# Performance work log

Hardware: AMD Instinct MI355X
Metric: run time of the kernel (lower is better)

## Reference

```python
import jax, jax.numpy as jnp
import numpy as np
from jax import lax

D = 1024      # d_model
NH = 16       # n_head
CA = 384      # adapter_channels
T = 16        # num_frames
B = 4         # videos
L = 257       # tokens = 16*16 patches + CLS
HW = 16       # spatial side


def setup_inputs() -> dict:
    key = jax.random.key(0)
    ks = jax.random.split(key, 12)
    s = 0.02
    f = lambda k, shp: jax.random.normal(k, shp, jnp.float32) * s
    return {
        'x': jax.random.normal(ks[0], (B * T, L, D), jnp.float32),
        'ln1_g': jnp.ones((D,), jnp.float32), 'ln1_b': jnp.zeros((D,), jnp.float32),
        'w_in': f(ks[1], (3 * D, D)), 'b_in': jnp.zeros((3 * D,), jnp.float32),
        'w_out': f(ks[2], (D, D)), 'b_out': jnp.zeros((D,), jnp.float32),
        'o_fc1_w': f(ks[3], (CA, D)), 'o_fc1_b': jnp.zeros((CA,), jnp.float32),
        'o_conv_w': f(ks[4], (3, 3, 1, CA)), 'o_conv_b': jnp.zeros((CA,), jnp.float32),
        'o_fc2_w': f(ks[5], (D, CA)), 'o_fc2_b': jnp.zeros((D,), jnp.float32),
        'a_fc1_w': f(ks[6], (CA, D)), 'a_fc1_b': jnp.zeros((CA,), jnp.float32),
        'a_conv_w': f(ks[7], (3, 1, CA)), 'a_conv_b': jnp.zeros((CA,), jnp.float32),
        'a_fc2_w': f(ks[8], (D, CA)), 'a_fc2_b': jnp.zeros((D,), jnp.float32),
        'ln2_g': jnp.ones((D,), jnp.float32), 'ln2_b': jnp.zeros((D,), jnp.float32),
        'mlp_fc_w': f(ks[9], (4 * D, D)), 'mlp_fc_b': jnp.zeros((4 * D,), jnp.float32),
        'mlp_proj_w': f(ks[10], (D, 4 * D)), 'mlp_proj_b': jnp.zeros((D,), jnp.float32),
    }


def _ln(x, g, b):
    # fp32 LayerNorm (matches CLIP LayerNorm subclass)
    x32 = x.astype(jnp.float32)
    mu = jnp.mean(x32, -1, keepdims=True)
    var = jnp.mean(jnp.square(x32 - mu), -1, keepdims=True)
    return ((x32 - mu) * lax.rsqrt(var + 1e-5) * g + b).astype(x.dtype)


def _mha(x, w_in, b_in, w_out, b_out):
    BT, Lq, C = x.shape
    hd = C // NH
    qkv = x @ w_in.T + b_in                       # (BT, L, 3C)
    q, k, v = jnp.split(qkv, 3, axis=-1)
    sh = lambda t: t.reshape(BT, Lq, NH, hd).transpose(0, 2, 1, 3)  # (BT, H, L, hd)
    q, k, v = sh(q), sh(k), sh(v)
    scores = jnp.einsum('bhqd,bhkd->bhqk', q * (hd ** -0.5), k)
    attn = jax.nn.softmax(scores, axis=-1)
    out = jnp.einsum('bhqk,bhkd->bhqd', attn, v)
    out = out.transpose(0, 2, 1, 3).reshape(BT, Lq, C)
    return out @ w_out.T + b_out


def _offset_adapter(x, fc1_w, fc1_b, conv_w, conv_b, fc2_w, fc2_b):
    BT, Lx, C = x.shape
    Bv = BT // T
    xs = x[:, 1:, :].reshape(Bv, T, Lx - 1, C)          # drop CLS
    former = jnp.concatenate([xs[:, :1], xs[:, :-1]], axis=1)
    off = xs - former                                    # temporal diff
    off = off @ fc1_w.T + fc1_b                          # (B, T, HW*HW, Ca)
    off = off.reshape(Bv * T, HW, HW, CA)
    # depthwise (1,3,3) Conv3d: kernel size 1 along T -> per-frame 3x3 depthwise conv
    off = lax.conv_general_dilated(off, conv_w, (1, 1), [(1, 1), (1, 1)],
                                   dimension_numbers=('NHWC', 'HWIO', 'NHWC'),
                                   feature_group_count=CA) + conv_b
    off = off.reshape(BT, Lx - 1, CA)
    return off @ fc2_w.T + fc2_b                         # (BT, L-1, C)


def _adapter2(x, a_fc1_w, a_fc1_b, a_conv_w, a_conv_b, a_fc2_w, a_fc2_b,
              o_fc1_w, o_fc1_b, o_conv_w, o_conv_b, o_fc2_w, o_fc2_b):
    BT, Lx, C = x.shape
    Bv = BT // T
    off = _offset_adapter(x, o_fc1_w, o_fc1_b, o_conv_w, o_conv_b, o_fc2_w, o_fc2_b)
    y = x @ a_fc1_w.T + a_fc1_b                          # (BT, L, Ca)
    y = y.reshape(Bv, T, Lx, CA).transpose(0, 2, 1, 3).reshape(Bv * Lx, T, CA)
    # depthwise Conv1d along the temporal axis
    y = lax.conv_general_dilated(y, a_conv_w, (1,), [(1, 1)],
                                 dimension_numbers=('NWC', 'WIO', 'NWC'),
                                 feature_group_count=CA) + a_conv_b
    y = y.reshape(Bv, Lx, T, CA).transpose(0, 2, 1, 3).reshape(BT, Lx, CA)
    y = y @ a_fc2_w.T + a_fc2_b                          # (BT, L, C)
    x_id = x.at[:, 1:, :].add(off)
    return y + x_id


def _block(x, ln1_g, ln1_b, w_in, b_in, w_out, b_out,
           a_fc1_w, a_fc1_b, a_conv_w, a_conv_b, a_fc2_w, a_fc2_b,
           o_fc1_w, o_fc1_b, o_conv_w, o_conv_b, o_fc2_w, o_fc2_b,
           ln2_g, ln2_b, mlp_fc_w, mlp_fc_b, mlp_proj_w, mlp_proj_b):
    x = x + _mha(_ln(x, ln1_g, ln1_b), w_in, b_in, w_out, b_out)
    x = _adapter2(x, a_fc1_w, a_fc1_b, a_conv_w, a_conv_b, a_fc2_w, a_fc2_b,
                  o_fc1_w, o_fc1_b, o_conv_w, o_conv_b, o_fc2_w, o_fc2_b)
    h = _ln(x, ln2_g, ln2_b) @ mlp_fc_w.T + mlp_fc_b
    h = h * jax.nn.sigmoid(1.702 * h)                    # QuickGELU
    return x + h @ mlp_proj_w.T + mlp_proj_b


def reference(x, ln1_g, ln1_b, w_in, b_in, w_out, b_out,
              o_fc1_w, o_fc1_b, o_conv_w, o_conv_b, o_fc2_w, o_fc2_b,
              a_fc1_w, a_fc1_b, a_conv_w, a_conv_b, a_fc2_w, a_fc2_b,
              ln2_g, ln2_b, mlp_fc_w, mlp_fc_b, mlp_proj_w, mlp_proj_b):
    return _block(x, ln1_g, ln1_b, w_in, b_in, w_out, b_out,
                  a_fc1_w, a_fc1_b, a_conv_w, a_conv_b, a_fc2_w, a_fc2_b,
                  o_fc1_w, o_fc1_b, o_conv_w, o_conv_b, o_fc2_w, o_fc2_b,
                  ln2_g, ln2_b, mlp_fc_w, mlp_fc_b, mlp_proj_w, mlp_proj_b)
```

## Files before the change

kernel.cpp:

```cpp
#include <hip/hip_runtime.h>
#include <cstdint>
#include <cstddef>


typedef unsigned short u16;
typedef __attribute__((ext_vector_type(4))) float  f32x4;
typedef __attribute__((ext_vector_type(8))) short  bf16x8;
typedef __attribute__((ext_vector_type(4))) unsigned int u32x4;

#define AS1 __attribute__((address_space(1)))
#define AS3 __attribute__((address_space(3)))

__device__ __forceinline__ float bf2f(u16 u) {
  unsigned int x = ((unsigned int)u) << 16;
  return __builtin_bit_cast(float, x);
}
__device__ __forceinline__ u16 f2bf(float f) {
  unsigned int x = __builtin_bit_cast(unsigned int, f);
  x = x + 0x7fffu + ((x >> 16) & 1u);
  return (u16)(x >> 16);
}
__device__ __forceinline__ unsigned int pack2(float a, float b) {
  return (unsigned int)f2bf(a) | ((unsigned int)f2bf(b) << 16);
}
__device__ __forceinline__ int imin(int a, int b) { return a < b ? a : b; }

__device__ __forceinline__ void gload_lds16(const void* g, void* l) {
  __builtin_amdgcn_global_load_lds((const AS1 unsigned int*)g,
                                   (AS3 unsigned int*)l, 16, 0, 0);
}

__global__ __launch_bounds__(256) void cvt_weights(
    const float* __restrict__ w_in, const float* __restrict__ w_out,
    const float* __restrict__ ofc1, const float* __restrict__ ofc2,
    const float* __restrict__ afc1, const float* __restrict__ afc2,
    const float* __restrict__ mfc,  const float* __restrict__ mproj,
    u16* __restrict__ dst)
{
  long i4 = (long)blockIdx.x * 256 + threadIdx.x;
  long e = i4 * 4;
  const float* src; long base;
  if      (e < 3145728L) { src = w_in;  base = 0L; }
  else if (e < 4194304L) { src = w_out; base = 3145728L; }
  else if (e < 4587520L) { src = ofc1;  base = 4194304L; }
  else if (e < 4980736L) { src = ofc2;  base = 4587520L; }
  else if (e < 5373952L) { src = afc1;  base = 4980736L; }
  else if (e < 5767168L) { src = afc2;  base = 5373952L; }
  else if (e < 9961472L) { src = mfc;   base = 5767168L; }
  else                   { src = mproj; base = 9961472L; }
  float4 v = *(const float4*)(src + (e - base));
  uint2 o; o.x = pack2(v.x, v.y); o.y = pack2(v.z, v.w);
  *(uint2*)(dst + e) = o;
}

__global__ __launch_bounds__(256) void ln_bf16(
    const float* __restrict__ x, const float* __restrict__ g,
    const float* __restrict__ b, u16* __restrict__ out)
{
  int row = blockIdx.x;
  const float4* xr = (const float4*)(x + (size_t)row * 1024);
  float4 v = xr[threadIdx.x];
  float s = v.x + v.y + v.z + v.w;
  float q = v.x * v.x + v.y * v.y + v.z * v.z + v.w * v.w;
  #pragma unroll
  for (int m = 1; m < 64; m <<= 1) { s += __shfl_xor(s, m); q += __shfl_xor(q, m); }
  __shared__ float ss[4], qq[4];
  if ((threadIdx.x & 63) == 0) { ss[threadIdx.x >> 6] = s; qq[threadIdx.x >> 6] = q; }
  __syncthreads();
  s = ss[0] + ss[1] + ss[2] + ss[3];
  q = qq[0] + qq[1] + qq[2] + qq[3];
  float mu = s * (1.f / 1024.f);
  float var = q * (1.f / 1024.f) - mu * mu;
  float rs = rsqrtf(var + 1e-5f);
  float4 gg = ((const float4*)g)[threadIdx.x];
  float4 bb = ((const float4*)b)[threadIdx.x];
  float o0 = (v.x - mu) * rs * gg.x + bb.x;
  float o1 = (v.y - mu) * rs * gg.y + bb.y;
  float o2 = (v.z - mu) * rs * gg.z + bb.z;
  float o3 = (v.w - mu) * rs * gg.w + bb.w;
  uint2 o; o.x = pack2(o0, o1); o.y = pack2(o2, o3);
  *(uint2*)(out + (size_t)row * 1024 + threadIdx.x * 4) = o;
}

__global__ __launch_bounds__(256) void diff_bf16(
    const float* __restrict__ x1, u16* __restrict__ out)
{
  int i = blockIdx.x * 256 + threadIdx.x;
  int r = i >> 8;
  int c4 = i & 255;
  int f = r >> 8;
  int p = r & 255;
  int t = f & 15;
  int rowA = f * 257 + 1 + p;
  int rowB = (t == 0) ? rowA : (f - 1) * 257 + 1 + p;
  float4 a = ((const float4*)(x1 + (size_t)rowA * 1024))[c4];
  float4 b = ((const float4*)(x1 + (size_t)rowB * 1024))[c4];
  uint2 o; o.x = pack2(a.x - b.x, a.y - b.y); o.y = pack2(a.z - b.z, a.w - b.w);
  *(uint2*)(out + (size_t)r * 1024 + c4 * 4) = o;
}

__global__ __launch_bounds__(256) void dwconv3x3(
    const u16* __restrict__ in, const float* __restrict__ w,
    const float* __restrict__ bias, u16* __restrict__ out)
{
  int idx = blockIdx.x * 256 + threadIdx.x;
  int c = idx % 384;
  int pos = idx / 384;
  int xx = pos & 15, yy = (pos >> 4) & 15, f = pos >> 8;
  float acc = bias[c];
  #pragma unroll
  for (int kh = 0; kh < 3; kh++) {
    int y2 = yy + kh - 1;
    if (y2 < 0 || y2 > 15) continue;
    #pragma unroll
    for (int kw = 0; kw < 3; kw++) {
      int x2 = xx + kw - 1;
      if (x2 < 0 || x2 > 15) continue;
      acc += bf2f(in[((size_t)(f * 256 + y2 * 16 + x2)) * 384 + c]) * w[(kh * 3 + kw) * 384 + c];
    }
  }
  out[(size_t)idx] = f2bf(acc);
}

__global__ __launch_bounds__(256) void dwconv1d(
    const u16* __restrict__ in, const float* __restrict__ w,
    const float* __restrict__ bias, u16* __restrict__ out)
{
  int idx = blockIdx.x * 256 + threadIdx.x;
  int c = idx % 384;
  int rl = idx / 384;
  int bt = rl / 257, l = rl % 257;
  int bv = bt >> 4, t = bt & 15;
  float acc = bias[c];
  #pragma unroll
  for (int dt = 0; dt < 3; dt++) {
    int tt = t + dt - 1;
    if (tt < 0 || tt > 15) continue;
    acc += bf2f(in[((size_t)((bv * 16 + tt) * 257 + l)) * 384 + c]) * w[dt * 384 + c];
  }
  out[(size_t)idx] = f2bf(acc);
}

enum { EPI_BF16 = 0, EPI_GELU = 1, EPI_RES = 2, EPI_ACC = 3, EPI_ACC_SKIPCLS = 4 };

template <int EPI>
__global__ __launch_bounds__(256) void gemm_bt(
    const u16* __restrict__ A, const u16* __restrict__ B,
    const float* __restrict__ bias,
    float* __restrict__ outF, u16* __restrict__ outB,
    const float* __restrict__ resid,
    int M, int N, int K)
{
  __shared__ u16 As[128 * 64];
  __shared__ u16 Bs[128 * 64];
  const int t = threadIdx.x, l = t & 63, w = t >> 6;
  const int row0 = blockIdx.x * 128, col0 = blockIdx.y * 128;
  const int wr = w >> 1, wc = w & 1;
  const int lo = l & 15, hi = l >> 4;
  const int larow = l >> 3, lacol = (l & 7) * 8;

  f32x4 acc[4][4];
  const f32x4 z = {0.f, 0.f, 0.f, 0.f};
  #pragma unroll
  for (int m = 0; m < 4; m++)
    #pragma unroll
    for (int n = 0; n < 4; n++) acc[m][n] = z;

  for (int k0 = 0; k0 < K; k0 += 64) {
    #pragma unroll
    for (int i = 0; i < 4; i++) {
      int rr = i * 32 + w * 8 + larow;
      int ra = row0 + rr; ra = (ra < M) ? ra : (M - 1);
      gload_lds16(A + (size_t)ra * K + k0 + lacol, As + i * 2048 + w * 512);
      gload_lds16(B + (size_t)(col0 + rr) * K + k0 + lacol, Bs + i * 2048 + w * 512);
    }
    __syncthreads();
    #pragma unroll
    for (int kk = 0; kk < 2; kk++) {
      bf16x8 af[4], bfr[4];
      #pragma unroll
      for (int m = 0; m < 4; m++)
        af[m] = __builtin_bit_cast(bf16x8,
          *(const u32x4*)&As[(wr * 64 + m * 16 + lo) * 64 + kk * 32 + hi * 8]);
      #pragma unroll
      for (int n = 0; n < 4; n++)
        bfr[n] = __builtin_bit_cast(bf16x8,
          *(const u32x4*)&Bs[(wc * 64 + n * 16 + lo) * 64 + kk * 32 + hi * 8]);
      #pragma unroll
      for (int m = 0; m < 4; m++)
        #pragma unroll
        for (int n = 0; n < 4; n++)
          acc[m][n] = __builtin_amdgcn_mfma_f32_16x16x32_bf16(af[m], bfr[n], acc[m][n], 0, 0, 0);
    }
    __syncthreads();
  }

  const int rbase = row0 + wr * 64, cbase = col0 + wc * 64;
  #pragma unroll
  for (int n = 0; n < 4; n++) {
    int colc = cbase + n * 16 + lo;
    float bv = bias[colc];
    #pragma unroll
    for (int m = 0; m < 4; m++) {
      int rr0 = rbase + m * 16 + hi * 4;
      #pragma unroll
      for (int j = 0; j < 4; j++) {
        int r = rr0 + j;
        if (r >= M) continue;
        float v = acc[m][n][j] + bv;
        if constexpr (EPI == EPI_BF16) {
          outB[(size_t)r * N + colc] = f2bf(v);
        } else if constexpr (EPI == EPI_GELU) {
          float gv = v / (1.f + __expf(-1.702f * v));
          outB[(size_t)r * N + colc] = f2bf(gv);
        } else if constexpr (EPI == EPI_RES) {
          float sres = resid[(size_t)r * N + colc] + v;
          outF[(size_t)r * N + colc] = sres;
          outB[(size_t)r * N + colc] = f2bf(sres);
        } else if constexpr (EPI == EPI_ACC) {
          outF[(size_t)r * N + colc] += v;
        } else {
          int rm = (r >> 8) * 257 + (r & 255) + 1;
          outF[(size_t)rm * N + colc] += v;
        }
      }
    }
  }
}

template <int EPI>
__global__ __launch_bounds__(512, 2) void gemm256(
    const u16* __restrict__ A, const u16* __restrict__ B,
    const float* __restrict__ bias,
    float* __restrict__ outF, u16* __restrict__ outB,
    const float* __restrict__ resid,
    int M, int N, int K, int gm)
{
  __shared__ u16 lds[65536];
  const int tid = threadIdx.x;
  const int w = tid >> 6, lane = tid & 63;
  const int lo = lane & 15, hi = lane >> 4;
  const int wm = w >> 2, wn = w & 3;

  const int nwg = gridDim.x, orig = blockIdx.x;
  const int q = nwg >> 3, r = nwg & 7;
  const int xcd = orig & 7, jj = orig >> 3;
  const int lid = (xcd < r ? xcd * (q + 1) : r * (q + 1) + (xcd - r) * q) + jj;
  const int sg = lid / (gm * 4), rem = lid - sg * (gm * 4);
  const int tm = rem >> 2, tn = sg * 4 + (rem & 3);
  const int row0 = tm * 256, col0 = tn * 256;

  const int srow = w * 8 + (lane >> 3);
  const int scolEl = ((lane & 7) ^ (lane >> 3)) << 3;
  const u16* aS[4]; const u16* bS[4];
  #pragma unroll
  for (int i = 0; i < 4; i++) {
    int ar = imin(row0 + i * 64 + srow, M - 1);
    aS[i] = A + (size_t)ar * K + scolEl;
    bS[i] = B + (size_t)(col0 + i * 64 + srow) * K + scolEl;
  }
  auto stageA = [&](int c2, int kOff) {
    u16* d = (u16*)lds + c2 * 32768 + (w << 9);
    #pragma unroll
    for (int i = 0; i < 4; i++) gload_lds16(aS[i] + kOff, d + i * 4096);
  };
  auto stageB = [&](int c2, int kOff) {
    u16* d = (u16*)lds + c2 * 32768 + 16384 + (w << 9);
    #pragma unroll
    for (int i = 0; i < 4; i++) gload_lds16(bS[i] + kOff, d + i * 4096);
  };

  const int swz = (lo & 7) << 3;
  const int cK0 = (hi << 3) ^ swz;
  const int cK1 = ((hi << 3) | 32) ^ swz;
  const int aRowE = (wm * 128 + lo) * 64;
  const int bRowE = (wn * 64 + lo) * 64;

  f32x4 acc[8][4];
  const f32x4 z = {0.f, 0.f, 0.f, 0.f};
  #pragma unroll
  for (int m = 0; m < 8; m++)
    #pragma unroll
    for (int n = 0; n < 4; n++) acc[m][n] = z;

  bf16x8 aF[4][2], bF0[2][2], bF1[2][2];

#define LOADA(BA, MH)                                                          \
  { _Pragma("unroll")                                                          \
    for (int mi = 0; mi < 4; mi++) {                                           \
      const u16* p = (BA) + aRowE + ((MH) * 4 + mi) * 1024;                    \
      aF[mi][0] = __builtin_bit_cast(bf16x8, *(const u32x4*)(p + cK0));        \
      aF[mi][1] = __builtin_bit_cast(bf16x8, *(const u32x4*)(p + cK1));        \
    } }
#define LOADB(BB, BF, NH)                                                      \
  { _Pragma("unroll")                                                          \
    for (int ni = 0; ni < 2; ni++) {                                           \
      const u16* p = (BB) + bRowE + ((NH) * 2 + ni) * 1024;                    \
      BF[ni][0] = __builtin_bit_cast(bf16x8, *(const u32x4*)(p + cK0));        \
      BF[ni][1] = __builtin_bit_cast(bf16x8, *(const u32x4*)(p + cK1));        \
    } }
#define MFMA16(MH, NH, BF)                                                     \
  { _Pragma("unroll")                                                          \
    for (int mi = 0; mi < 4; mi++)                                             \
      _Pragma("unroll")                                                        \
      for (int ni = 0; ni < 2; ni++)                                           \
        _Pragma("unroll")                                                      \
        for (int kk = 0; kk < 2; kk++)                                         \
          acc[(MH)*4+mi][(NH)*2+ni] = __builtin_amdgcn_mfma_f32_16x16x32_bf16( \
              aF[mi][kk], BF[ni][kk], acc[(MH)*4+mi][(NH)*2+ni], 0, 0, 0); }

  const int NT = K >> 6;
  stageA(0, 0);
  stageB(0, 0);
  asm volatile("s_waitcnt vmcnt(0)" ::: "memory");
  __builtin_amdgcn_s_barrier();

  for (int t = 0; t < NT; ++t) {
    const int c = t & 1;
    const u16* bufA = (const u16*)lds + c * 32768;
    const u16* bufB = bufA + 16384;
    const bool pf = (t + 1) < NT;
    const int kn = (t + 1) << 6;

    LOADA(bufA, 0);
    LOADB(bufB, bF0, 0);
    if (pf) stageA(c ^ 1, kn);
    __builtin_amdgcn_sched_barrier(0);
    __builtin_amdgcn_s_barrier();
    __builtin_amdgcn_s_setprio(1);
    MFMA16(0, 0, bF0);
    __builtin_amdgcn_s_setprio(0);
    __builtin_amdgcn_sched_barrier(0);
    __builtin_amdgcn_s_barrier();
    LOADB(bufB, bF1, 1);
    if (pf) stageB(c ^ 1, kn);
    __builtin_amdgcn_sched_barrier(0);
    __builtin_amdgcn_s_barrier();
    __builtin_amdgcn_s_setprio(1);
    MFMA16(0, 1, bF1);
    __builtin_amdgcn_s_setprio(0);
    __builtin_amdgcn_sched_barrier(0);
    __builtin_amdgcn_s_barrier();
    LOADA(bufA, 1);
    __builtin_amdgcn_sched_barrier(0);
    __builtin_amdgcn_s_barrier();
    __builtin_amdgcn_s_setprio(1);
    MFMA16(1, 1, bF1);
    __builtin_amdgcn_s_setprio(0);
    __builtin_amdgcn_sched_barrier(0);
    __builtin_amdgcn_s_barrier();
    __builtin_amdgcn_s_setprio(1);
    MFMA16(1, 0, bF0);
    __builtin_amdgcn_s_setprio(0);
    __builtin_amdgcn_sched_barrier(0);
    asm volatile("s_waitcnt vmcnt(0)" ::: "memory");
    __builtin_amdgcn_s_barrier();
  }
#undef LOADA
#undef LOADB
#undef MFMA16

  const int rbase = row0 + wm * 128, cbase = col0 + wn * 64;
  #pragma unroll
  for (int n = 0; n < 4; n++) {
    int colc = cbase + n * 16 + lo;
    float bvv = bias[colc];
    #pragma unroll
    for (int m = 0; m < 8; m++) {
      int rr0 = rbase + m * 16 + hi * 4;
      #pragma unroll
      for (int j = 0; j < 4; j++) {
        int rr = rr0 + j;
        if (rr >= M) continue;
        float v = acc[m][n][j] + bvv;
        if constexpr (EPI == EPI_BF16) {
          outB[(size_t)rr * N + colc] = f2bf(v);
        } else if constexpr (EPI == EPI_GELU) {
          float gv = v / (1.f + __expf(-1.702f * v));
          outB[(size_t)rr * N + colc] = f2bf(gv);
        } else if constexpr (EPI == EPI_RES) {
          float sres = resid[(size_t)rr * N + colc] + v;
          outF[(size_t)rr * N + colc] = sres;
          outB[(size_t)rr * N + colc] = f2bf(sres);
        } else if constexpr (EPI == EPI_ACC) {
          outF[(size_t)rr * N + colc] += v;
        } else {
          int rm = (rr >> 8) * 257 + (rr & 255) + 1;
          outF[(size_t)rm * N + colc] += v;
        }
      }
    }
  }
}

__global__ __launch_bounds__(256) void attn_kernel(
    const u16* __restrict__ qkv, u16* __restrict__ out)
{
  __shared__ u16 Vt[64 * 296];
  __shared__ u16 Ps[4][16 * 136];
  const int bt = blockIdx.x >> 4;
  const int h  = blockIdx.x & 15;
  const int t  = threadIdx.x, l = t & 63, w = t >> 6;
  const int lo = l & 15, hi = l >> 4;
  const size_t base = (size_t)bt * 257 * 3072 + (size_t)h * 64;

  for (int ch = t; ch < 257 * 8; ch += 256) {
    int r = ch >> 3, s8 = ch & 7;
    u32x4 v = *(const u32x4*)(qkv + base + (size_t)r * 3072 + 2048 + s8 * 8);
    union { u32x4 v4; u16 us[8]; } cv; cv.v4 = v;
    #pragma unroll
    for (int i = 0; i < 8; i++) Vt[(s8 * 8 + i) * 296 + r] = cv.us[i];
  }
  for (int ch = t; ch < 64 * 39; ch += 256)
    Vt[(ch / 39) * 296 + 257 + (ch % 39)] = 0;
  __syncthreads();

  for (int c = w; c < 17; c += 4) {
    int qr = c * 16 + lo; qr = (qr < 257) ? qr : 256;
    const u16* qp = qkv + base + (size_t)qr * 3072 + hi * 8;
    bf16x8 q0 = __builtin_bit_cast(bf16x8, *(const u32x4*)qp);
    bf16x8 q1 = __builtin_bit_cast(bf16x8, *(const u32x4*)(qp + 32));

    f32x4 s[17];
    #pragma unroll
    for (int tt = 0; tt < 17; tt++) {
      int kr = tt * 16 + lo; kr = (kr < 257) ? kr : 256;
      const u16* kp = qkv + base + (size_t)kr * 3072 + 1024 + hi * 8;
      bf16x8 k0 = __builtin_bit_cast(bf16x8, *(const u32x4*)kp);
      bf16x8 k1 = __builtin_bit_cast(bf16x8, *(const u32x4*)(kp + 32));
      f32x4 a = {0.f, 0.f, 0.f, 0.f};
      a = __builtin_amdgcn_mfma_f32_16x16x32_bf16(q0, k0, a, 0, 0, 0);
      a = __builtin_amdgcn_mfma_f32_16x16x32_bf16(q1, k1, a, 0, 0, 0);
      s[tt] = a;
    }
    float mx[4] = {-1e30f, -1e30f, -1e30f, -1e30f};
    #pragma unroll
    for (int tt = 0; tt < 17; tt++) {
      int key = tt * 16 + lo;
      #pragma unroll
      for (int j = 0; j < 4; j++) {
        float v = s[tt][j] * 0.125f;
        v = (key < 257) ? v : -1e30f;
        s[tt][j] = v;
        mx[j] = fmaxf(mx[j], v);
      }
    }
    #pragma unroll
    for (int j = 0; j < 4; j++)
      #pragma unroll
      for (int msk = 1; msk < 16; msk <<= 1) mx[j] = fmaxf(mx[j], __shfl_xor(mx[j], msk));
    float sm[4] = {0.f, 0.f, 0.f, 0.f};
    #pragma unroll
    for (int tt = 0; tt < 17; tt++)
      #pragma unroll
      for (int j = 0; j < 4; j++) {
        float p = __expf(s[tt][j] - mx[j]);
        s[tt][j] = p; sm[j] += p;
      }
    #pragma unroll
    for (int j = 0; j < 4; j++) {
      #pragma unroll
      for (int msk = 1; msk < 16; msk <<= 1) sm[j] += __shfl_xor(sm[j], msk);
      sm[j] = 1.f / sm[j];
    }

    u16* P = &Ps[w][0];
    f32x4 o[4];
    #pragma unroll
    for (int n = 0; n < 4; n++) o[n] = (f32x4){0.f, 0.f, 0.f, 0.f};
    #pragma unroll
    for (int ph = 0; ph < 3; ph++) {
      const int TT = (ph < 2) ? 8 : 1;
      #pragma unroll
      for (int ti = 0; ti < TT; ti++) {
        int tt = ph * 8 + ti;
        #pragma unroll
        for (int j = 0; j < 4; j++)
          P[(hi * 4 + j) * 136 + ti * 16 + lo] = f2bf(s[tt][j] * sm[j]);
      }
      if (ph == 2) {
        #pragma unroll
        for (int j = 0; j < 4; j++) P[(hi * 4 + j) * 136 + 16 + lo] = 0;
      }
      const int NKS = (ph < 2) ? 4 : 1;
      #pragma unroll
      for (int ks = 0; ks < NKS; ks++) {
        bf16x8 af = __builtin_bit_cast(bf16x8,
          *(const u32x4*)&P[lo * 136 + ks * 32 + hi * 8]);
        #pragma unroll
        for (int n = 0; n < 4; n++) {
          bf16x8 bfr = __builtin_bit_cast(bf16x8,
            *(const u32x4*)&Vt[(n * 16 + lo) * 296 + ph * 128 + ks * 32 + hi * 8]);
          o[n] = __builtin_amdgcn_mfma_f32_16x16x32_bf16(af, bfr, o[n], 0, 0, 0);
        }
      }
    }
    #pragma unroll
    for (int n = 0; n < 4; n++)
      #pragma unroll
      for (int j = 0; j < 4; j++) {
        int row = c * 16 + hi * 4 + j;
        if (row < 257)
          out[(size_t)(bt * 257 + row) * 1024 + h * 64 + n * 16 + lo] = f2bf(o[n][j]);
      }
  }
}

extern "C" void kernel_launch(void* const* d_in, const int* in_sizes, int n_in,
                              void* d_out, int out_size, void* d_ws, size_t ws_size,
                              hipStream_t stream)
{
  const float* x       = (const float*)d_in[0];
  const float* ln1_g   = (const float*)d_in[1];
  const float* ln1_b   = (const float*)d_in[2];
  const float* w_in    = (const float*)d_in[3];
  const float* b_in    = (const float*)d_in[4];
  const float* w_out   = (const float*)d_in[5];
  const float* b_out   = (const float*)d_in[6];
  const float* o_fc1_w = (const float*)d_in[7];
  const float* o_fc1_b = (const float*)d_in[8];
  const float* o_conv_w= (const float*)d_in[9];
  const float* o_conv_b= (const float*)d_in[10];
  const float* o_fc2_w = (const float*)d_in[11];
  const float* o_fc2_b = (const float*)d_in[12];
  const float* a_fc1_w = (const float*)d_in[13];
  const float* a_fc1_b = (const float*)d_in[14];
  const float* a_conv_w= (const float*)d_in[15];
  const float* a_conv_b= (const float*)d_in[16];
  const float* a_fc2_w = (const float*)d_in[17];
  const float* a_fc2_b = (const float*)d_in[18];
  const float* ln2_g   = (const float*)d_in[19];
  const float* ln2_b   = (const float*)d_in[20];
  const float* mfc_w   = (const float*)d_in[21];
  const float* mfc_b   = (const float*)d_in[22];
  const float* mproj_w = (const float*)d_in[23];
  const float* mproj_b = (const float*)d_in[24];
  float* xo = (float*)d_out;

  char* ws = (char*)d_ws;
  u16* WB = (u16*)ws;
  u16* R0 = (u16*)(ws + 28311552);
  u16* R1 = (u16*)(ws + 28311552 + 33685504);
  u16* R2 = (u16*)(ws + 28311552 + 33685504 + 101056512);
  u16* w_in_bf  = WB + 0;
  u16* w_out_bf = WB + 3145728;
  u16* ofc1_bf  = WB + 4194304;
  u16* ofc2_bf  = WB + 4587520;
  u16* afc1_bf  = WB + 4980736;
  u16* afc2_bf  = WB + 5373952;
  u16* mfc_bf   = WB + 5767168;
  u16* mproj_bf = WB + 9961472;
  u16* off1 = R1;
  u16* offc = R1 + 6291456;
  u16* y1   = R1 + 12582912;
  u16* yc   = R1 + 12582912 + 6316032;

  cvt_weights<<<13824, 256, 0, stream>>>(w_in, w_out, o_fc1_w, o_fc2_w,
                                         a_fc1_w, a_fc2_w, mfc_w, mproj_w, WB);
  ln_bf16<<<16448, 256, 0, stream>>>(x, ln1_g, ln1_b, R0);
  gemm256<EPI_BF16><<<65 * 12, 512, 0, stream>>>(
      R0, w_in_bf, b_in, nullptr, R1, nullptr, 16448, 3072, 1024, 65);
  attn_kernel<<<1024, 256, 0, stream>>>(R1, R2);
  gemm256<EPI_RES><<<65 * 4, 512, 0, stream>>>(
      R2, w_out_bf, b_out, xo, R0, x, 16448, 1024, 1024, 65);
  diff_bf16<<<16384, 256, 0, stream>>>(xo, R2);
  gemm_bt<EPI_BF16><<<dim3(128, 3), 256, 0, stream>>>(
      R2, ofc1_bf, o_fc1_b, nullptr, off1, nullptr, 16384, 384, 1024);
  dwconv3x3<<<24576, 256, 0, stream>>>(off1, o_conv_w, o_conv_b, offc);
  gemm256<EPI_ACC_SKIPCLS><<<64 * 4, 512, 0, stream>>>(
      offc, ofc2_bf, o_fc2_b, xo, nullptr, nullptr, 16384, 1024, 384, 64);
  gemm_bt<EPI_BF16><<<dim3(129, 3), 256, 0, stream>>>(
      R0, afc1_bf, a_fc1_b, nullptr, y1, nullptr, 16448, 384, 1024);
  dwconv1d<<<24672, 256, 0, stream>>>(y1, a_conv_w, a_conv_b, yc);
  gemm256<EPI_ACC><<<65 * 4, 512, 0, stream>>>(
      yc, afc2_bf, a_fc2_b, xo, nullptr, nullptr, 16448, 1024, 384, 65);
  ln_bf16<<<16448, 256, 0, stream>>>(xo, ln2_g, ln2_b, R0);
  gemm256<EPI_GELU><<<65 * 16, 512, 0, stream>>>(
      R0, mfc_bf, mfc_b, nullptr, R1, nullptr, 16448, 4096, 1024, 65);
  gemm256<EPI_ACC><<<65 * 4, 512, 0, stream>>>(
      R1, mproj_bf, mproj_b, xo, nullptr, nullptr, 16448, 1024, 4096, 65);
}
```

Baseline: 1.473 ms.

## Switch GEMM main loop to four-stage K=32 LDS pipeline with deeper prefetch

Reworks the 256x256 GEMM mainloop from a double-buffered K=64 tile into a four-slot ring of K=32 tiles, keeping three tiles in flight via global-to-LDS loads and partial vmcnt waits. The LDS layout, swizzle and fragment loads are rewritten for 32-wide rows, and each iteration now runs two MFMA phases instead of four. The aim is to hide global memory latency better and cut barriers per K element. In exchange there are twice as many loop iterations, and the wait-count bookkeeping gets more fragile.

```diff
diff --git a/kernel.cpp b/kernel.cpp
--- a/kernel.cpp
+++ b/kernel.cpp
@@ -250,31 +250,31 @@
   const int tm = rem >> 2, tn = sg * 4 + (rem & 3);
   const int row0 = tm * 256, col0 = tn * 256;
 
-  const int srow = w * 8 + (lane >> 3);
-  const int scolEl = ((lane & 7) ^ (lane >> 3)) << 3;
-  const u16* aS[4]; const u16* bS[4];
-  #pragma unroll
-  for (int i = 0; i < 4; i++) {
-    int ar = imin(row0 + i * 64 + srow, M - 1);
-    aS[i] = A + (size_t)ar * K + scolEl;
-    bS[i] = B + (size_t)(col0 + i * 64 + srow) * K + scolEl;
-  }
-  auto stageA = [&](int c2, int kOff) {
-    u16* d = (u16*)lds + c2 * 32768 + (w << 9);
-    #pragma unroll
-    for (int i = 0; i < 4; i++) gload_lds16(aS[i] + kOff, d + i * 4096);
+  const int srow = w * 16 + (lane >> 2);
+  const int scolEl = (((lane & 3) ^ ((lane >> 3) & 3)) << 3);
+  const u16* aS0 = A + (size_t)imin(row0 + srow, M - 1) * K + scolEl;
+  const u16* aS1 = A + (size_t)imin(row0 + 128 + srow, M - 1) * K + scolEl;
+  const u16* bS0 = B + (size_t)(col0 + srow) * K + scolEl;
+  const u16* bS1 = B + (size_t)(col0 + 128 + srow) * K + scolEl;
+  u16* ldsp = (u16*)lds;
+  const int wOff = w << 9;
+
+  auto stageA = [&](int kt) {
+    u16* d = ldsp + (kt & 3) * 16384 + wOff;
+    const int k0 = kt << 5;
+    gload_lds16(aS0 + k0, d);
+    gload_lds16(aS1 + k0, d + 4096);
   };
-  auto stageB = [&](int c2, int kOff) {
-    u16* d = (u16*)lds + c2 * 32768 + 16384 + (w << 9);
-    #pragma unroll
-    for (int i = 0; i < 4; i++) gload_lds16(bS[i] + kOff, d + i * 4096);
+  auto stageB = [&](int kt) {
+    u16* d = ldsp + (kt & 3) * 16384 + 8192 + wOff;
+    const int k0 = kt << 5;
+    gload_lds16(bS0 + k0, d);
+    gload_lds16(bS1 + k0, d + 4096);
   };
 
-  const int swz = (lo & 7) << 3;
-  const int cK0 = (hi << 3) ^ swz;
-  const int cK1 = ((hi << 3) | 32) ^ swz;
-  const int aRowE = (wm * 128 + lo) * 64;
-  const int bRowE = (wn * 64 + lo) * 64;
+  const int cK = ((hi ^ ((lo >> 1) & 3)) << 3);
+  const int aRowE = (wm * 128 + lo) * 32;
+  const int bRowE = (wn * 64 + lo) * 32;
 
   f32x4 acc[8][4];
   const f32x4 z = {0.f, 0.f, 0.f, 0.f};
@@ -283,78 +283,66 @@
     #pragma unroll
     for (int n = 0; n < 4; n++) acc[m][n] = z;
 
-  bf16x8 aF[4][2], bF0[2][2], bF1[2][2];
+  bf16x8 aF[4], bF[4];
 
 #define LOADA(BA, MH)                                                          \
   { _Pragma("unroll")                                                          \
-    for (int mi = 0; mi < 4; mi++) {                                           \
-      const u16* p = (BA) + aRowE + ((MH) * 4 + mi) * 1024;                    \
-      aF[mi][0] = __builtin_bit_cast(bf16x8, *(const u32x4*)(p + cK0));        \
-      aF[mi][1] = __builtin_bit_cast(bf16x8, *(const u32x4*)(p + cK1));        \
-    } }
-#define LOADB(BB, BF, NH)                                                      \
+    for (int mi = 0; mi < 4; mi++)                                             \
+      aF[mi] = __builtin_bit_cast(bf16x8,                                      \
+        *(const u32x4*)((BA) + aRowE + ((MH) * 4 + mi) * 512 + cK)); }
+#define LOADB(BB)                                                              \
   { _Pragma("unroll")                                                          \
-    for (int ni = 0; ni < 2; ni++) {                                           \
-      const u16* p = (BB) + bRowE + ((NH) * 2 + ni) * 1024;                    \
-      BF[ni][0] = __builtin_bit_cast(bf16x8, *(const u32x4*)(p + cK0));        \
-      BF[ni][1] = __builtin_bit_cast(bf16x8, *(const u32x4*)(p + cK1));        \
-    } }
-#define MFMA16(MH, NH, BF)                                                     \
+    for (int ni = 0; ni < 4; ni++)                                             \
+      bF[ni] = __builtin_bit_cast(bf16x8,                                      \
+        *(const u32x4*)((BB) + bRowE + ni * 512 + cK)); }
+#define MFMA16(MH)                                                             \
   { _Pragma("unroll")                                                          \
     for (int mi = 0; mi < 4; mi++)                                             \
       _Pragma("unroll")                                                        \
-      for (int ni = 0; ni < 2; ni++)                                           \
-        _Pragma("unroll")                                                      \
-        for (int kk = 0; kk < 2; kk++)                                         \
-          acc[(MH)*4+mi][(NH)*2+ni] = __builtin_amdgcn_mfma_f32_16x16x32_bf16( \
-              aF[mi][kk], BF[ni][kk], acc[(MH)*4+mi][(NH)*2+ni], 0, 0, 0); }
-
-  const int NT = K >> 6;
-  stageA(0, 0);
-  stageB(0, 0);
-  asm volatile("s_waitcnt vmcnt(0)" ::: "memory");
+      for (int ni = 0; ni < 4; ni++)                                           \
+        acc[(MH)*4+mi][ni] = __builtin_amdgcn_mfma_f32_16x16x32_bf16(          \
+            aF[mi], bF[ni], acc[(MH)*4+mi][ni], 0, 0, 0); }
+
+  const int NT = K >> 5;
+  stageA(0); stageB(0);
+  stageA(1); stageB(1);
+  stageA(2); stageB(2);
+  asm volatile("s_waitcnt vmcnt(8)" ::: "memory");
   __builtin_amdgcn_s_barrier();
 
   for (int t = 0; t < NT; ++t) {
-    const int c = t & 1;
-    const u16* bufA = (const u16*)lds + c * 32768;
-    const u16* bufB = bufA + 16384;
-    const bool pf = (t + 1) < NT;
-    const int kn = (t + 1) << 6;
-
+    const u16* bufA = ldsp + (t & 3) * 16384;
+    const u16* bufB = bufA + 8192;
+    const bool pf = (t + 3) < NT;
+
+    LOADB(bufB);
     LOADA(bufA, 0);
-    LOADB(bufB, bF0, 0);
-    if (pf) stageA(c ^ 1, kn);
+    if (pf) stageA(t + 3);
     __builtin_amdgcn_sched_barrier(0);
     __builtin_amdgcn_s_barrier();
     __builtin_amdgcn_s_setprio(1);
-    MFMA16(0, 0, bF0);
-    __builtin_amdgcn_s_setprio(0);
-    __builtin_amdgcn_sched_barrier(0);
-    __builtin_amdgcn_s_barrier();
-    LOADB(bufB, bF1, 1);
-    if (pf) stageB(c ^ 1, kn);
-    __builtin_amdgcn_sched_barrier(0);
-    __builtin_amdgcn_s_barrier();
-    __builtin_amdgcn_s_setprio(1);
-    MFMA16(0, 1, bF1);
+    MFMA16(0);
     __builtin_amdgcn_s_setprio(0);
     __builtin_amdgcn_sched_barrier(0);
     __builtin_amdgcn_s_barrier();
     LOADA(bufA, 1);
+    if (pf) stageB(t + 3);
     __builtin_amdgcn_sched_barrier(0);
     __builtin_amdgcn_s_barrier();
     __builtin_amdgcn_s_setprio(1);
-    MFMA16(1, 1, bF1);
+    MFMA16(1);
     __builtin_amdgcn_s_setprio(0);
     __builtin_amdgcn_sched_barrier(0);
-    __builtin_amdgcn_s_barrier();
-    __builtin_amdgcn_s_setprio(1);
-    MFMA16(1, 0, bF0);
-    __builtin_amdgcn_s_setprio(0);
-    __builtin_amdgcn_sched_barrier(0);
-    asm volatile("s_waitcnt vmcnt(0)" ::: "memory");
-    __builtin_amdgcn_s_barrier();
+    if (t + 3 < NT) {
+      asm volatile("s_waitcnt vmcnt(8)" ::: "memory");
+      __builtin_amdgcn_s_barrier();
+    } else if (t + 2 < NT) {
+      asm volatile("s_waitcnt vmcnt(4)" ::: "memory");
+      __builtin_amdgcn_s_barrier();
+    } else if (t + 1 < NT) {
+      asm volatile("s_waitcnt vmcnt(0)" ::: "memory");
+      __builtin_amdgcn_s_barrier();
+    }
   }
 #undef LOADA
 #undef LOADB
```

Result: slower. 1.505 ms (+2.2%).
